# Optimization experiments

Hardware: AMD Instinct MI355X
Metric: run time of the kernel (lower is better)

The kernel has to match this reference:

```python
import jax, jax.numpy as jnp
import numpy as np

N, MAXO, IN_DIM = 4096, 16, 512
RNN_UNITS = (512, 512)
COMM_UNITS = (512, 256)
SIG = COMM_UNITS[-1]
COMM_IN = SIG + 5 + RNN_UNITS[-1]  # signal + one-hot(4) + dist + tiled features


def _lstm(x, h, c, Wx, Wh, b):
    # Keras LSTMCell gate order: i, f, g(candidate), o
    z = x @ Wx + h @ Wh + b
    i, f, g, o = jnp.split(z, 4, axis=-1)
    c2 = jax.nn.sigmoid(f) * c + jax.nn.sigmoid(i) * jnp.tanh(g)
    h2 = jax.nn.sigmoid(o) * jnp.tanh(c2)
    return h2, c2


def _mk_lstm(key, in_dim, units, scale=0.05):
    k1, k2, k3 = jax.random.split(key, 3)
    Wx = scale * jax.random.normal(k1, (in_dim, 4 * units), dtype=jnp.float32)
    Wh = scale * jax.random.normal(k2, (units, 4 * units), dtype=jnp.float32)
    b = scale * jax.random.normal(k3, (4 * units,), dtype=jnp.float32)
    return Wx, Wh, b


def setup_inputs():
    key = jax.random.key(0)
    ks = jax.random.split(key, 18)
    inputs = jax.random.normal(ks[0], (N, IN_DIM), dtype=jnp.float32)
    # interleaved triples (agent_id in [-1,N), dist, dir in [0,4))
    ids = jax.random.randint(ks[1], (N, MAXO), -1, N)
    dists = jax.random.randint(ks[2], (N, MAXO), 0, 20)
    dirs = jax.random.randint(ks[3], (N, MAXO), 0, 4)
    present_indices = jnp.stack([ids, dists, dirs], axis=2).reshape(N, 3 * MAXO).astype(jnp.int32)

    s = lambda k, shape: 0.05 * jax.random.normal(k, shape, dtype=jnp.float32)
    inp = dict(
        inputs=inputs, present_indices=present_indices,
        rnn_h1=s(ks[4], (N, RNN_UNITS[0])), rnn_c1=s(ks[5], (N, RNN_UNITS[0])),
        rnn_h2=s(ks[6], (N, RNN_UNITS[1])), rnn_c2=s(ks[7], (N, RNN_UNITS[1])),
        comm_h1=s(ks[8], (N, COMM_UNITS[0])), comm_c1=s(ks[9], (N, COMM_UNITS[0])),
        comm_h2=s(ks[10], (N, COMM_UNITS[1])), comm_c2=s(ks[11], (N, COMM_UNITS[1])),
        signals=s(ks[12], (N, SIG)),
    )
    inp['Wx1'], inp['Wh1'], inp['b1'] = _mk_lstm(ks[13], IN_DIM, RNN_UNITS[0])
    inp['Wx2'], inp['Wh2'], inp['b2'] = _mk_lstm(ks[14], RNN_UNITS[0], RNN_UNITS[1])
    inp['CWx1'], inp['CWh1'], inp['Cb1'] = _mk_lstm(ks[15], COMM_IN, COMM_UNITS[0])
    inp['CWx2'], inp['CWh2'], inp['Cb2'] = _mk_lstm(ks[16], COMM_UNITS[0], COMM_UNITS[1])
    return inp


def _forward(inputs, present_indices,
             rnn_h1, rnn_c1, rnn_h2, rnn_c2,
             comm_h1, comm_c1, comm_h2, comm_c2, signals,
             Wx1, Wh1, b1, Wx2, Wh2, b2,
             CWx1, CWh1, Cb1, CWx2, CWh2, Cb2):
    n = inputs.shape[0]
    # inner stacked LSTM step; features = output of last layer
    h1, c1 = _lstm(inputs, rnn_h1, rnn_c1, Wx1, Wh1, b1)
    h2, c2 = _lstm(h1, rnn_h2, rnn_c2, Wx2, Wh2, b2)
    features = h2  # [n, RNN_UNITS[-1]]

    vis_dists = present_indices[:, 1::3].astype(jnp.float32)      # [n, MAXO]
    vis_dirs = present_indices[:, 2::3]                            # [n, MAXO]
    pres = present_indices[:, 0::3]                                # [n, MAXO]
    dirs_onehot = jax.nn.one_hot(vis_dirs, 4, dtype=jnp.float32)   # [n, MAXO, 4]

    # append self at the end of the neighbor sequence
    pres = jnp.concatenate([pres, jnp.arange(n, dtype=pres.dtype)[:, None]], axis=1)  # [n, T]
    vis_dists = jnp.pad(vis_dists, ((0, 0), (0, 1)))
    dirs_onehot = jnp.pad(dirs_onehot, ((0, 0), (0, 1), (0, 0)))

    # _gather_present: zero row for absent (-1) neighbors
    padded_signals = jnp.pad(signals, ((1, 0), (0, 0)))            # [n+1, SIG]
    gathered = padded_signals[pres + 1]                            # [n, T, SIG]
    mask = pres >= 0                                               # [n, T]

    T = pres.shape[1]
    sig_in = jnp.concatenate([
        gathered,
        dirs_onehot,
        vis_dists[:, :, None],
        jnp.broadcast_to(features[:, None, :], (n, T, features.shape[-1])),
    ], axis=2)                                                     # [n, T, COMM_IN]

    # masked stacked-LSTM scan over the neighbor axis (Keras RNN mask semantics:
    # masked steps carry states and previous output through)
    xs = (jnp.swapaxes(sig_in, 0, 1), jnp.swapaxes(mask, 0, 1))

    def step(carry, xm):
        ch1, cc1, ch2, cc2, lo = carry
        xt, mt = xm
        nh1, nc1 = _lstm(xt, ch1, cc1, CWx1, CWh1, Cb1)
        nh2, nc2 = _lstm(nh1, ch2, cc2, CWx2, CWh2, Cb2)
        m = mt[:, None]
        carry = (jnp.where(m, nh1, ch1), jnp.where(m, nc1, cc1),
                 jnp.where(m, nh2, ch2), jnp.where(m, nc2, cc2),
                 jnp.where(m, nh2, lo))
        return carry, None

    init = (comm_h1, comm_c1, comm_h2, comm_c2, jnp.zeros_like(comm_h2))
    (nch1, ncc1, nch2, ncc2, out_signals), _ = jax.lax.scan(step, init, xs)

    full_output = jnp.concatenate([out_signals, out_signals, features], axis=1)
    return full_output


def reference(inputs, present_indices,
              rnn_h1, rnn_c1, rnn_h2, rnn_c2,
              comm_h1, comm_c1, comm_h2, comm_c2, signals,
              Wx1, Wh1, b1, Wx2, Wh2, b2,
              CWx1, CWh1, Cb1, CWx2, CWh2, Cb2):
    return _forward(inputs, present_indices,
                    rnn_h1, rnn_c1, rnn_h2, rnn_c2,
                    comm_h1, comm_c1, comm_h2, comm_c2, signals,
                    Wx1, Wh1, b1, Wx2, Wh2, b2,
                    CWx1, CWh1, Cb1, CWx2, CWh2, Cb2)
```

## Files before the change

### kernel.cpp

```cpp
#include <hip/hip_runtime.h>
#include <initializer_list>
#include <cstdint>
#include <cstddef>


typedef short short8 __attribute__((ext_vector_type(8)));
typedef float f32x4 __attribute__((ext_vector_type(4)));
typedef unsigned short us;

#define N_AG 4096

__device__ __forceinline__ us f2bf(float x) {
  unsigned int u = __float_as_uint(x);
  unsigned int r = (u + 0x7fffu + ((u >> 16) & 1u)) >> 16;
  return (us)r;
}
__device__ __forceinline__ float sigm(float x) { return 1.f / (1.f + __expf(-x)); }
__device__ __forceinline__ float tanh_f(float x) {
  float e = __expf(2.f * x);
  return 1.f - 2.f / (1.f + e);
}

struct Pair { const us* A; const us* B; int K; };
struct GemmArgs { Pair pr[6]; int np; int N; const float* base; int mode; float* C; };

typedef __attribute__((address_space(1))) const unsigned int as1u;
typedef __attribute__((address_space(3))) unsigned int as3u;
__device__ __forceinline__ void gload16(const void* g, void* l) {
  __builtin_amdgcn_global_load_lds((as1u*)g, (as3u*)l, 16, 0, 0);
}

__global__ __launch_bounds__(256) void k_gemm(GemmArgs g) {
  __shared__ __align__(16) us lA[128 * 32];
  __shared__ __align__(16) us lB[128 * 32];
  const int t = threadIdx.x;
  const int w = t >> 6, l = t & 63;
  const int bm = blockIdx.y, bn = blockIdx.x;
  const int wm = w & 1, wn = w >> 1;
  const int fr = l & 15, ks = l >> 4;
  const int srow = t >> 2;
  const int sslot = (t & 3) ^ ((srow >> 1) & 3);
  f32x4 acc[4][4] = {};

  for (int p = 0; p < g.np; ++p) {
    const us* A = g.pr[p].A;
    const us* B = g.pr[p].B;
    const int K = g.pr[p].K;
    const us* Ab = A + (size_t)bm * 128 * K;
    const us* Bb = B + (size_t)bn * 128 * K;
    for (int k0 = 0; k0 < K; k0 += 32) {
      __syncthreads();
#pragma unroll
      for (int r = 0; r < 2; ++r) {
        const int row = srow + r * 64;
        gload16(Ab + (size_t)row * K + k0 + sslot * 8, (char*)lA + r * 4096 + w * 1024);
        gload16(Bb + (size_t)row * K + k0 + sslot * 8, (char*)lB + r * 4096 + w * 1024);
      }
      __syncthreads();
      short8 af[4], bfr[4];
#pragma unroll
      for (int mi = 0; mi < 4; ++mi) {
        const int row = wm * 64 + mi * 16 + fr;
        af[mi] = *(const short8*)((const char*)lA + row * 64 + ((ks ^ ((row >> 1) & 3)) * 16));
      }
#pragma unroll
      for (int ni = 0; ni < 4; ++ni) {
        const int row = wn * 64 + ni * 16 + fr;
        bfr[ni] = *(const short8*)((const char*)lB + row * 64 + ((ks ^ ((row >> 1) & 3)) * 16));
      }
#pragma unroll
      for (int mi = 0; mi < 4; ++mi)
#pragma unroll
        for (int ni = 0; ni < 4; ++ni)
          acc[mi][ni] = __builtin_amdgcn_mfma_f32_16x16x32_bf16(af[mi], bfr[ni], acc[mi][ni], 0, 0, 0);
    }
  }
  const int N = g.N;
#pragma unroll
  for (int mi = 0; mi < 4; ++mi) {
#pragma unroll
    for (int ni = 0; ni < 4; ++ni) {
#pragma unroll
      for (int rr = 0; rr < 4; ++rr) {
        const int grow = bm * 128 + wm * 64 + mi * 16 + ks * 4 + rr;
        const int gcol = bn * 128 + wn * 64 + ni * 16 + fr;
        float v = acc[mi][ni][rr];
        if (g.mode == 1) v += g.base[gcol];
        else if (g.mode == 2) v += g.base[(size_t)grow * N + gcol];
        g.C[(size_t)grow * N + gcol] = v;
      }
    }
  }
}

__global__ __launch_bounds__(256) void k_transpose(const float* __restrict__ src,
    int Nout, int Kreal, int Kpad, int roff, us* __restrict__ dst) {
  int idx = blockIdx.x * 256 + threadIdx.x;
  if (idx >= Nout * Kpad) return;
  int no = idx % Nout;
  int k = idx / Nout;
  float v = (k < Kreal) ? src[(size_t)(roff + k) * Nout + no] : 0.f;
  dst[(size_t)no * Kpad + k] = f2bf(v);
}

__global__ __launch_bounds__(256) void k_split(const float* __restrict__ src, int n,
    float* __restrict__ f, us* __restrict__ b) {
  int idx = blockIdx.x * 256 + threadIdx.x;
  if (idx >= n) return;
  float v = src[idx];
  if (f) f[idx] = v;
  if (b) b[idx] = f2bf(v);
}

__global__ __launch_bounds__(256) void k_xvar(const int* __restrict__ pi,
    const float* __restrict__ sig, int t, us* __restrict__ xb) {
  int idx = blockIdx.x * 256 + threadIdx.x;
  if (idx >= N_AG * 288) return;
  int n = idx / 288, c = idx - n * 288;
  float v = 0.f;
  if (t < 16) {
    int p = pi[n * 48 + 3 * t];
    if (c < 256) v = (p >= 0) ? sig[(size_t)p * 256 + c] : 0.f;
    else if (c < 260) v = ((c - 256) == pi[n * 48 + 3 * t + 2]) ? 1.f : 0.f;
    else if (c == 260) v = (float)pi[n * 48 + 3 * t + 1];
  } else {
    if (c < 256) v = sig[(size_t)n * 256 + c];
  }
  xb[idx] = f2bf(v);
}

__global__ __launch_bounds__(256) void k_ew_simple(const float* __restrict__ Z,
    const float* __restrict__ cin, float* __restrict__ hf, us* __restrict__ hb) {
  int idx = blockIdx.x * 256 + threadIdx.x;
  if (idx >= N_AG * 512) return;
  int n = idx >> 9, u = idx & 511;
  const float* zr = Z + (size_t)n * 2048;
  float nc = sigm(zr[512 + u]) * cin[idx] + sigm(zr[u]) * tanh_f(zr[1024 + u]);
  float nh = sigm(zr[1536 + u]) * tanh_f(nc);
  if (hf) hf[idx] = nh;
  hb[idx] = f2bf(nh);
}

__global__ __launch_bounds__(256) void k_ew_comm1(const float* __restrict__ Z,
    const int* __restrict__ pi, int t, float* __restrict__ h, float* __restrict__ c,
    us* __restrict__ hb, us* __restrict__ nhb) {
  int idx = blockIdx.x * 256 + threadIdx.x;
  if (idx >= N_AG * 512) return;
  int n = idx >> 9, u = idx & 511;
  const float* zr = Z + (size_t)n * 2048;
  float cold = c[idx];
  float nc = sigm(zr[512 + u]) * cold + sigm(zr[u]) * tanh_f(zr[1024 + u]);
  float nh = sigm(zr[1536 + u]) * tanh_f(nc);
  bool m = (t == 16) ? true : (pi[n * 48 + 3 * t] >= 0);
  float hn = m ? nh : h[idx];
  float cn = m ? nc : cold;
  h[idx] = hn;
  c[idx] = cn;
  hb[idx] = f2bf(hn);
  nhb[idx] = f2bf(nh);
}

__global__ __launch_bounds__(256) void k_ew_comm2(const float* __restrict__ Z,
    const int* __restrict__ pi, int t, float* __restrict__ h, float* __restrict__ c,
    us* __restrict__ hb) {
  int idx = blockIdx.x * 256 + threadIdx.x;
  if (idx >= N_AG * 256) return;
  int n = idx >> 8, u = idx & 255;
  const float* zr = Z + (size_t)n * 1024;
  float cold = c[idx];
  float nc = sigm(zr[256 + u]) * cold + sigm(zr[u]) * tanh_f(zr[512 + u]);
  float nh = sigm(zr[768 + u]) * tanh_f(nc);
  bool m = (t == 16) ? true : (pi[n * 48 + 3 * t] >= 0);
  float hn = m ? nh : h[idx];
  float cn = m ? nc : cold;
  h[idx] = hn;
  c[idx] = cn;
  hb[idx] = f2bf(hn);
}

__global__ __launch_bounds__(256) void k_out(const float* __restrict__ h2,
    const float* __restrict__ feat, float* __restrict__ out) {
  int idx = blockIdx.x * 256 + threadIdx.x;
  if (idx >= N_AG * 1024) return;
  int n = idx >> 10, cc = idx & 1023;
  out[idx] = (cc < 512) ? h2[(size_t)n * 256 + (cc & 255)] : feat[(size_t)n * 512 + cc - 512];
}

extern "C" void kernel_launch(void* const* d_in, const int* in_sizes, int n_in,
                              void* d_out, int out_size, void* d_ws, size_t ws_size,
                              hipStream_t stream) {
  const float* inputs  = (const float*)d_in[0];
  const int*   pres    = (const int*)d_in[1];
  const float* rnn_h1  = (const float*)d_in[2];
  const float* rnn_c1  = (const float*)d_in[3];
  const float* rnn_h2  = (const float*)d_in[4];
  const float* rnn_c2  = (const float*)d_in[5];
  const float* comm_h1 = (const float*)d_in[6];
  const float* comm_c1 = (const float*)d_in[7];
  const float* comm_h2 = (const float*)d_in[8];
  const float* comm_c2 = (const float*)d_in[9];
  const float* signals = (const float*)d_in[10];
  const float* Wx1 = (const float*)d_in[11];
  const float* Wh1 = (const float*)d_in[12];
  const float* b1  = (const float*)d_in[13];
  const float* Wx2 = (const float*)d_in[14];
  const float* Wh2 = (const float*)d_in[15];
  const float* b2  = (const float*)d_in[16];
  const float* CWx1 = (const float*)d_in[17];
  const float* CWh1 = (const float*)d_in[18];
  const float* Cb1  = (const float*)d_in[19];
  const float* CWx2 = (const float*)d_in[20];
  const float* CWh2 = (const float*)d_in[21];
  const float* Cb2  = (const float*)d_in[22];
  float* out = (float*)d_out;
  (void)in_sizes; (void)n_in; (void)out_size;

  char* wsb = (char*)d_ws;
  size_t off = 0;
  auto alloc = [&](size_t bytes) -> char* {
    char* p = wsb + off;
    off = (off + bytes + 255) & ~(size_t)255;
    return p;
  };
  us* wx1t = (us*)alloc(2048 * 512 * 2);
  us* wh1t = (us*)alloc(2048 * 512 * 2);
  us* wx2t = (us*)alloc(2048 * 512 * 2);
  us* wh2t = (us*)alloc(2048 * 512 * 2);
  us* cx1vt = (us*)alloc(2048 * 288 * 2);
  us* cx1ft = (us*)alloc(2048 * 512 * 2);
  us* ch1t = (us*)alloc(2048 * 512 * 2);
  us* cx2t = (us*)alloc(1024 * 512 * 2);
  us* ch2t = (us*)alloc(1024 * 256 * 2);
  us* in_b  = (us*)alloc(4096 * 512 * 2);
  us* rh1_b = (us*)alloc(4096 * 512 * 2);
  us* rh2_b = (us*)alloc(4096 * 512 * 2);
  us* h1p_b = (us*)alloc(4096 * 512 * 2);
  us* ft_b  = (us*)alloc(4096 * 512 * 2);
  us* h1_b  = (us*)alloc(4096 * 512 * 2);
  us* nh1_b = (us*)alloc(4096 * 512 * 2);
  us* h2_b  = (us*)alloc(4096 * 256 * 2);
  us* xv_b  = (us*)alloc(4096 * 288 * 2);
  float* feat = (float*)alloc(4096 * 512 * 4);
  float* F1 = (float*)alloc((size_t)4096 * 2048 * 4);
  float* Z1 = (float*)alloc((size_t)4096 * 2048 * 4);
  float* Z2 = (float*)alloc((size_t)4096 * 1024 * 4);
  float* h1 = (float*)alloc(4096 * 512 * 4);
  float* c1 = (float*)alloc(4096 * 512 * 4);
  float* h2 = (float*)alloc(4096 * 256 * 4);
  float* c2 = (float*)alloc(4096 * 256 * 4);
  if (off > ws_size) return;

  auto tsp = [&](const float* src, int Nout, int Kreal, int Kpad, int roff, us* dst) {
    int tot = Nout * Kpad;
    k_transpose<<<dim3((tot + 255) / 256), dim3(256), 0, stream>>>(src, Nout, Kreal, Kpad, roff, dst);
  };
  tsp(Wx1, 2048, 512, 512, 0, wx1t);
  tsp(Wh1, 2048, 512, 512, 0, wh1t);
  tsp(Wx2, 2048, 512, 512, 0, wx2t);
  tsp(Wh2, 2048, 512, 512, 0, wh2t);
  tsp(CWx1, 2048, 261, 288, 0, cx1vt);
  tsp(CWx1, 2048, 512, 512, 261, cx1ft);
  tsp(CWh1, 2048, 512, 512, 0, ch1t);
  tsp(CWx2, 1024, 512, 512, 0, cx2t);
  tsp(CWh2, 1024, 256, 256, 0, ch2t);

  auto spl = [&](const float* src, int n, float* f, us* b) {
    k_split<<<dim3((n + 255) / 256), dim3(256), 0, stream>>>(src, n, f, b);
  };
  spl(inputs, 4096 * 512, nullptr, in_b);
  spl(rnn_h1, 4096 * 512, nullptr, rh1_b);
  spl(rnn_h2, 4096 * 512, nullptr, rh2_b);
  spl(comm_h1, 4096 * 512, h1, h1_b);
  spl(comm_c1, 4096 * 512, c1, nullptr);
  spl(comm_h2, 4096 * 256, h2, h2_b);
  spl(comm_c2, 4096 * 256, c2, nullptr);

  auto gemm = [&](std::initializer_list<Pair> ps, int Ncols, const float* base, int mode, float* C) {
    GemmArgs ga{};
    int i = 0;
    for (auto& p : ps) ga.pr[i++] = p;
    ga.np = i; ga.N = Ncols; ga.base = base; ga.mode = mode; ga.C = C;
    k_gemm<<<dim3(Ncols / 128, 4096 / 128), dim3(256), 0, stream>>>(ga);
  };

  gemm({{in_b, wx1t, 512}, {rh1_b, wh1t, 512}}, 2048, b1, 1, Z1);
  k_ew_simple<<<dim3(4096 * 512 / 256), dim3(256), 0, stream>>>(Z1, rnn_c1, nullptr, h1p_b);
  gemm({{h1p_b, wx2t, 512}, {rh2_b, wh2t, 512}}, 2048, b2, 1, Z1);
  k_ew_simple<<<dim3(4096 * 512 / 256), dim3(256), 0, stream>>>(Z1, rnn_c2, feat, ft_b);
  gemm({{ft_b, cx1ft, 512}}, 2048, Cb1, 1, F1);

  for (int t = 0; t < 17; ++t) {
    k_xvar<<<dim3((4096 * 288 + 255) / 256), dim3(256), 0, stream>>>(pres, signals, t, xv_b);
    gemm({{xv_b, cx1vt, 288}, {h1_b, ch1t, 512}}, 2048, F1, 2, Z1);
    k_ew_comm1<<<dim3(4096 * 512 / 256), dim3(256), 0, stream>>>(Z1, pres, t, h1, c1, h1_b, nh1_b);
    gemm({{nh1_b, cx2t, 512}, {h2_b, ch2t, 256}}, 1024, Cb2, 1, Z2);
    k_ew_comm2<<<dim3(4096 * 256 / 256), dim3(256), 0, stream>>>(Z2, pres, t, h2, c2, h2_b);
  }
  k_out<<<dim3(4096 * 1024 / 256), dim3(256), 0, stream>>>(h2, feat, out);
}
```

Measured before the change: 1.869 ms.

## Fuse LSTM gate elementwise into GEMM epilogue with gate-interleaved weights

Reorders weight columns so each 64-column warp tile holds the i/f/g/o gates of the same 16 units. This lets the GEMM epilogue compute the LSTM cell update directly, which removes the separate elementwise kernels and the full fp32 Z buffer round trips. The GEMM K-step also grows from 32 to 64 with a wider swizzle, and the bf16 hidden-state buffers are double-buffered so blocks can read the old state while others write the new one. The variable-input K is padded to 320, which costs a little extra compute.

```diff
diff --git a/kernel.cpp b/kernel.cpp
--- a/kernel.cpp
+++ b/kernel.cpp
@@ -22,7 +22,19 @@
 }
 
 struct Pair { const us* A; const us* B; int K; };
-struct GemmArgs { Pair pr[6]; int np; int N; const float* base; int mode; float* C; };
+struct GemmArgs {
+  Pair pr[2]; int np; int N; int nunits;
+  const float* bias;
+  const float* base2;
+  const float* cin;
+  float* cout;
+  const float* hold;
+  float* hout;
+  us* hb;
+  us* nhb;
+  const int* pres; int tt;
+  float* C; int mode;
+};
 
 typedef __attribute__((address_space(1))) const unsigned int as1u;
 typedef __attribute__((address_space(3))) unsigned int as3u;
@@ -31,15 +43,13 @@
 }
 
 __global__ __launch_bounds__(256) void k_gemm(GemmArgs g) {
-  __shared__ __align__(16) us lA[128 * 32];
-  __shared__ __align__(16) us lB[128 * 32];
+  __shared__ __align__(16) us lA[128 * 64];
+  __shared__ __align__(16) us lB[128 * 64];
   const int t = threadIdx.x;
   const int w = t >> 6, l = t & 63;
   const int bm = blockIdx.y, bn = blockIdx.x;
   const int wm = w & 1, wn = w >> 1;
   const int fr = l & 15, ks = l >> 4;
-  const int srow = t >> 2;
-  const int sslot = (t & 3) ^ ((srow >> 1) & 3);
   f32x4 acc[4][4] = {};
 
   for (int p = 0; p < g.np; ++p) {
@@ -48,59 +58,96 @@
     const int K = g.pr[p].K;
     const us* Ab = A + (size_t)bm * 128 * K;
     const us* Bb = B + (size_t)bn * 128 * K;
-    for (int k0 = 0; k0 < K; k0 += 32) {
+    for (int k0 = 0; k0 < K; k0 += 64) {
       __syncthreads();
 #pragma unroll
-      for (int r = 0; r < 2; ++r) {
-        const int row = srow + r * 64;
-        gload16(Ab + (size_t)row * K + k0 + sslot * 8, (char*)lA + r * 4096 + w * 1024);
-        gload16(Bb + (size_t)row * K + k0 + sslot * 8, (char*)lB + r * 4096 + w * 1024);
+      for (int r0 = 0; r0 < 4; ++r0) {
+        const int srow = r0 * 32 + (t >> 3);
+        const int sslot = (t & 7) ^ (srow & 7);
+        gload16(Ab + (size_t)srow * K + k0 + sslot * 8, (char*)lA + r0 * 4096 + w * 1024);
+        gload16(Bb + (size_t)srow * K + k0 + sslot * 8, (char*)lB + r0 * 4096 + w * 1024);
       }
       __syncthreads();
-      short8 af[4], bfr[4];
-#pragma unroll
-      for (int mi = 0; mi < 4; ++mi) {
-        const int row = wm * 64 + mi * 16 + fr;
-        af[mi] = *(const short8*)((const char*)lA + row * 64 + ((ks ^ ((row >> 1) & 3)) * 16));
-      }
-#pragma unroll
-      for (int ni = 0; ni < 4; ++ni) {
-        const int row = wn * 64 + ni * 16 + fr;
-        bfr[ni] = *(const short8*)((const char*)lB + row * 64 + ((ks ^ ((row >> 1) & 3)) * 16));
-      }
-#pragma unroll
-      for (int mi = 0; mi < 4; ++mi)
-#pragma unroll
-        for (int ni = 0; ni < 4; ++ni)
-          acc[mi][ni] = __builtin_amdgcn_mfma_f32_16x16x32_bf16(af[mi], bfr[ni], acc[mi][ni], 0, 0, 0);
-    }
-  }
-  const int N = g.N;
-#pragma unroll
-  for (int mi = 0; mi < 4; ++mi) {
-#pragma unroll
-    for (int ni = 0; ni < 4; ++ni) {
-#pragma unroll
-      for (int rr = 0; rr < 4; ++rr) {
-        const int grow = bm * 128 + wm * 64 + mi * 16 + ks * 4 + rr;
-        const int gcol = bn * 128 + wn * 64 + ni * 16 + fr;
-        float v = acc[mi][ni][rr];
-        if (g.mode == 1) v += g.base[gcol];
-        else if (g.mode == 2) v += g.base[(size_t)grow * N + gcol];
-        g.C[(size_t)grow * N + gcol] = v;
+#pragma unroll
+      for (int kh = 0; kh < 2; ++kh) {
+        short8 af[4], bf[4];
+#pragma unroll
+        for (int mi = 0; mi < 4; ++mi) {
+          const int row = wm * 64 + mi * 16 + fr;
+          const int s = kh * 4 + ks;
+          af[mi] = *(const short8*)((const char*)lA + row * 128 + ((s ^ (row & 7)) << 4));
+        }
+#pragma unroll
+        for (int ni = 0; ni < 4; ++ni) {
+          const int row = wn * 64 + ni * 16 + fr;
+          const int s = kh * 4 + ks;
+          bf[ni] = *(const short8*)((const char*)lB + row * 128 + ((s ^ (row & 7)) << 4));
+        }
+#pragma unroll
+        for (int mi = 0; mi < 4; ++mi)
+#pragma unroll
+          for (int ni = 0; ni < 4; ++ni)
+            acc[mi][ni] = __builtin_amdgcn_mfma_f32_16x16x32_bf16(af[mi], bf[ni], acc[mi][ni], 0, 0, 0);
       }
     }
   }
+
+  const int N = g.N, nu = g.nunits;
+  const int u = (bn * 2 + wn) * 16 + fr;
+  if (g.mode == 0) {
+#pragma unroll
+    for (int mi = 0; mi < 4; ++mi)
+#pragma unroll
+      for (int ni = 0; ni < 4; ++ni)
+#pragma unroll
+        for (int rr = 0; rr < 4; ++rr) {
+          const int grow = bm * 128 + wm * 64 + mi * 16 + ks * 4 + rr;
+          const int col = bn * 128 + wn * 64 + ni * 16 + fr;
+          g.C[(size_t)grow * N + col] = acc[mi][ni][rr] + g.bias[ni * nu + u];
+        }
+    return;
+  }
+  float bi = 0.f, bfg = 0.f, bg = 0.f, bo = 0.f;
+  if (!g.base2) { bi = g.bias[u]; bfg = g.bias[nu + u]; bg = g.bias[2 * nu + u]; bo = g.bias[3 * nu + u]; }
+#pragma unroll
+  for (int mi = 0; mi < 4; ++mi) {
+#pragma unroll
+    for (int rr = 0; rr < 4; ++rr) {
+      const int grow = bm * 128 + wm * 64 + mi * 16 + ks * 4 + rr;
+      float zi = acc[mi][0][rr], zf = acc[mi][1][rr], zg = acc[mi][2][rr], zo = acc[mi][3][rr];
+      if (g.base2) {
+        const float* fb = g.base2 + (size_t)grow * N + bn * 128 + wn * 64 + fr;
+        zi += fb[0]; zf += fb[16]; zg += fb[32]; zo += fb[48];
+      } else {
+        zi += bi; zf += bfg; zg += bg; zo += bo;
+      }
+      const size_t off = (size_t)grow * nu + u;
+      const float cold = g.cin[off];
+      const float nc = sigm(zf) * cold + sigm(zi) * tanh_f(zg);
+      const float nh = sigm(zo) * tanh_f(nc);
+      bool m = true;
+      if (g.tt >= 0 && g.tt < 16) m = (g.pres[grow * 48 + 3 * g.tt] >= 0);
+      const float cn = m ? nc : cold;
+      float hn = nh;
+      if (g.hold) hn = m ? nh : g.hold[off];
+      if (g.cout) g.cout[off] = cn;
+      if (g.hout) g.hout[off] = hn;
+      g.hb[off] = f2bf(hn);
+      if (g.nhb) g.nhb[off] = f2bf(nh);
+    }
+  }
 }
 
 __global__ __launch_bounds__(256) void k_transpose(const float* __restrict__ src,
-    int Nout, int Kreal, int Kpad, int roff, us* __restrict__ dst) {
+    int Nout, int nunits, int Kreal, int Kpad, int roff, us* __restrict__ dst) {
   int idx = blockIdx.x * 256 + threadIdx.x;
   if (idx >= Nout * Kpad) return;
-  int no = idx % Nout;
+  int col = idx % Nout;
   int k = idx / Nout;
-  float v = (k < Kreal) ? src[(size_t)(roff + k) * Nout + no] : 0.f;
-  dst[(size_t)no * Kpad + k] = f2bf(v);
+  int gate = (col >> 4) & 3;
+  int u = ((col >> 6) << 4) | (col & 15);
+  float v = (k < Kreal) ? src[(size_t)(roff + k) * Nout + gate * nunits + u] : 0.f;
+  dst[(size_t)col * Kpad + k] = f2bf(v);
 }
 
 __global__ __launch_bounds__(256) void k_split(const float* __restrict__ src, int n,
@@ -115,8 +162,8 @@
 __global__ __launch_bounds__(256) void k_xvar(const int* __restrict__ pi,
     const float* __restrict__ sig, int t, us* __restrict__ xb) {
   int idx = blockIdx.x * 256 + threadIdx.x;
-  if (idx >= N_AG * 288) return;
-  int n = idx / 288, c = idx - n * 288;
+  if (idx >= N_AG * 320) return;
+  int n = idx / 320, c = idx - n * 320;
   float v = 0.f;
   if (t < 16) {
     int p = pi[n * 48 + 3 * t];
@@ -127,55 +174,6 @@
     if (c < 256) v = sig[(size_t)n * 256 + c];
   }
   xb[idx] = f2bf(v);
-}
-
-__global__ __launch_bounds__(256) void k_ew_simple(const float* __restrict__ Z,
-    const float* __restrict__ cin, float* __restrict__ hf, us* __restrict__ hb) {
-  int idx = blockIdx.x * 256 + threadIdx.x;
-  if (idx >= N_AG * 512) return;
-  int n = idx >> 9, u = idx & 511;
-  const float* zr = Z + (size_t)n * 2048;
-  float nc = sigm(zr[512 + u]) * cin[idx] + sigm(zr[u]) * tanh_f(zr[1024 + u]);
-  float nh = sigm(zr[1536 + u]) * tanh_f(nc);
-  if (hf) hf[idx] = nh;
-  hb[idx] = f2bf(nh);
-}
-
-__global__ __launch_bounds__(256) void k_ew_comm1(const float* __restrict__ Z,
-    const int* __restrict__ pi, int t, float* __restrict__ h, float* __restrict__ c,
-    us* __restrict__ hb, us* __restrict__ nhb) {
-  int idx = blockIdx.x * 256 + threadIdx.x;
-  if (idx >= N_AG * 512) return;
-  int n = idx >> 9, u = idx & 511;
-  const float* zr = Z + (size_t)n * 2048;
-  float cold = c[idx];
-  float nc = sigm(zr[512 + u]) * cold + sigm(zr[u]) * tanh_f(zr[1024 + u]);
-  float nh = sigm(zr[1536 + u]) * tanh_f(nc);
-  bool m = (t == 16) ? true : (pi[n * 48 + 3 * t] >= 0);
-  float hn = m ? nh : h[idx];
-  float cn = m ? nc : cold;
-  h[idx] = hn;
-  c[idx] = cn;
-  hb[idx] = f2bf(hn);
-  nhb[idx] = f2bf(nh);
-}
-
-__global__ __launch_bounds__(256) void k_ew_comm2(const float* __restrict__ Z,
-    const int* __restrict__ pi, int t, float* __restrict__ h, float* __restrict__ c,
-    us* __restrict__ hb) {
-  int idx = blockIdx.x * 256 + threadIdx.x;
-  if (idx >= N_AG * 256) return;
-  int n = idx >> 8, u = idx & 255;
-  const float* zr = Z + (size_t)n * 1024;
-  float cold = c[idx];
-  float nc = sigm(zr[256 + u]) * cold + sigm(zr[u]) * tanh_f(zr[512 + u]);
-  float nh = sigm(zr[768 + u]) * tanh_f(nc);
-  bool m = (t == 16) ? true : (pi[n * 48 + 3 * t] >= 0);
-  float hn = m ? nh : h[idx];
-  float cn = m ? nc : cold;
-  h[idx] = hn;
-  c[idx] = cn;
-  hb[idx] = f2bf(hn);
 }
 
 __global__ __launch_bounds__(256) void k_out(const float* __restrict__ h2,
@@ -222,28 +220,28 @@
     off = (off + bytes + 255) & ~(size_t)255;
     return p;
   };
-  us* wx1t = (us*)alloc(2048 * 512 * 2);
-  us* wh1t = (us*)alloc(2048 * 512 * 2);
-  us* wx2t = (us*)alloc(2048 * 512 * 2);
-  us* wh2t = (us*)alloc(2048 * 512 * 2);
-  us* cx1vt = (us*)alloc(2048 * 288 * 2);
+  us* wx1t  = (us*)alloc(2048 * 512 * 2);
+  us* wh1t  = (us*)alloc(2048 * 512 * 2);
+  us* wx2t  = (us*)alloc(2048 * 512 * 2);
+  us* wh2t  = (us*)alloc(2048 * 512 * 2);
+  us* cx1vt = (us*)alloc(2048 * 320 * 2);
   us* cx1ft = (us*)alloc(2048 * 512 * 2);
-  us* ch1t = (us*)alloc(2048 * 512 * 2);
-  us* cx2t = (us*)alloc(1024 * 512 * 2);
-  us* ch2t = (us*)alloc(1024 * 256 * 2);
-  us* in_b  = (us*)alloc(4096 * 512 * 2);
-  us* rh1_b = (us*)alloc(4096 * 512 * 2);
-  us* rh2_b = (us*)alloc(4096 * 512 * 2);
-  us* h1p_b = (us*)alloc(4096 * 512 * 2);
-  us* ft_b  = (us*)alloc(4096 * 512 * 2);
-  us* h1_b  = (us*)alloc(4096 * 512 * 2);
-  us* nh1_b = (us*)alloc(4096 * 512 * 2);
-  us* h2_b  = (us*)alloc(4096 * 256 * 2);
-  us* xv_b  = (us*)alloc(4096 * 288 * 2);
+  us* ch1t  = (us*)alloc(2048 * 512 * 2);
+  us* cx2t  = (us*)alloc(1024 * 512 * 2);
+  us* ch2t  = (us*)alloc(1024 * 256 * 2);
+  us* in_b   = (us*)alloc(4096 * 512 * 2);
+  us* rh1_b  = (us*)alloc(4096 * 512 * 2);
+  us* rh2_b  = (us*)alloc(4096 * 512 * 2);
+  us* h1p_b  = (us*)alloc(4096 * 512 * 2);
+  us* ft_b   = (us*)alloc(4096 * 512 * 2);
+  us* h1b0   = (us*)alloc(4096 * 512 * 2);
+  us* h1b1   = (us*)alloc(4096 * 512 * 2);
+  us* nh1_b  = (us*)alloc(4096 * 512 * 2);
+  us* h2b0   = (us*)alloc(4096 * 256 * 2);
+  us* h2b1   = (us*)alloc(4096 * 256 * 2);
+  us* xv_b   = (us*)alloc(4096 * 320 * 2);
   float* feat = (float*)alloc(4096 * 512 * 4);
-  float* F1 = (float*)alloc((size_t)4096 * 2048 * 4);
-  float* Z1 = (float*)alloc((size_t)4096 * 2048 * 4);
-  float* Z2 = (float*)alloc((size_t)4096 * 1024 * 4);
+  float* F1   = (float*)alloc((size_t)4096 * 2048 * 4);
   float* h1 = (float*)alloc(4096 * 512 * 4);
   float* c1 = (float*)alloc(4096 * 512 * 4);
   float* h2 = (float*)alloc(4096 * 256 * 4);
@@ -252,13 +250,13 @@
 
   auto tsp = [&](const float* src, int Nout, int Kreal, int Kpad, int roff, us* dst) {
     int tot = Nout * Kpad;
-    k_transpose<<<dim3((tot + 255) / 256), dim3(256), 0, stream>>>(src, Nout, Kreal, Kpad, roff, dst);
+    k_transpose<<<dim3((tot + 255) / 256), dim3(256), 0, stream>>>(src, Nout, Nout / 4, Kreal, Kpad, roff, dst);
   };
   tsp(Wx1, 2048, 512, 512, 0, wx1t);
   tsp(Wh1, 2048, 512, 512, 0, wh1t);
   tsp(Wx2, 2048, 512, 512, 0, wx2t);
   tsp(Wh2, 2048, 512, 512, 0, wh2t);
-  tsp(CWx1, 2048, 261, 288, 0, cx1vt);
+  tsp(CWx1, 2048, 261, 320, 0, cx1vt);
   tsp(CWx1, 2048, 512, 512, 261, cx1ft);
   tsp(CWh1, 2048, 512, 512, 0, ch1t);
   tsp(CWx2, 1024, 512, 512, 0, cx2t);
@@ -270,31 +268,50 @@
   spl(inputs, 4096 * 512, nullptr, in_b);
   spl(rnn_h1, 4096 * 512, nullptr, rh1_b);
   spl(rnn_h2, 4096 * 512, nullptr, rh2_b);
-  spl(comm_h1, 4096 * 512, h1, h1_b);
+  spl(comm_h1, 4096 * 512, h1, h1b0);
   spl(comm_c1, 4096 * 512, c1, nullptr);
-  spl(comm_h2, 4096 * 256, h2, h2_b);
+  spl(comm_h2, 4096 * 256, h2, h2b0);
   spl(comm_c2, 4096 * 256, c2, nullptr);
 
-  auto gemm = [&](std::initializer_list<Pair> ps, int Ncols, const float* base, int mode, float* C) {
+  auto launch = [&](GemmArgs& ga) {
+    k_gemm<<<dim3(ga.N / 128, 4096 / 128), dim3(256), 0, stream>>>(ga);
+  };
+  auto lstm = [&](std::initializer_list<Pair> ps, int Ncols, const float* bias, const float* base2,
+                  const float* cin, float* cout, const float* hold, float* hout,
+                  us* hb, us* nhb, const int* pm, int tt) {
     GemmArgs ga{};
     int i = 0;
     for (auto& p : ps) ga.pr[i++] = p;
-    ga.np = i; ga.N = Ncols; ga.base = base; ga.mode = mode; ga.C = C;
-    k_gemm<<<dim3(Ncols / 128, 4096 / 128), dim3(256), 0, stream>>>(ga);
-  };
-
-  gemm({{in_b, wx1t, 512}, {rh1_b, wh1t, 512}}, 2048, b1, 1, Z1);
-  k_ew_simple<<<dim3(4096 * 512 / 256), dim3(256), 0, stream>>>(Z1, rnn_c1, nullptr, h1p_b);
-  gemm({{h1p_b, wx2t, 512}, {rh2_b, wh2t, 512}}, 2048, b2, 1, Z1);
-  k_ew_simple<<<dim3(4096 * 512 / 256), dim3(256), 0, stream>>>(Z1, rnn_c2, feat, ft_b);
-  gemm({{ft_b, cx1ft, 512}}, 2048, Cb1, 1, F1);
-
+    ga.np = i; ga.N = Ncols; ga.nunits = Ncols / 4;
+    ga.bias = bias; ga.base2 = base2; ga.cin = cin; ga.cout = cout;
+    ga.hold = hold; ga.hout = hout; ga.hb = hb; ga.nhb = nhb;
+    ga.pres = pm; ga.tt = tt; ga.C = nullptr; ga.mode = 1;
+    launch(ga);
+  };
+  auto plain = [&](std::initializer_list<Pair> ps, int Ncols, const float* bias, float* C) {
+    GemmArgs ga{};
+    int i = 0;
+    for (auto& p : ps) ga.pr[i++] = p;
+    ga.np = i; ga.N = Ncols; ga.nunits = Ncols / 4;
+    ga.bias = bias; ga.C = C; ga.mode = 0; ga.tt = -1;
+    launch(ga);
+  };
+
+  lstm({{in_b, wx1t, 512}, {rh1_b, wh1t, 512}}, 2048, b1, nullptr,
+       rnn_c1, nullptr, nullptr, nullptr, h1p_b, nullptr, nullptr, -1);
+  lstm({{h1p_b, wx2t, 512}, {rh2_b, wh2t, 512}}, 2048, b2, nullptr,
+       rnn_c2, nullptr, nullptr, feat, ft_b, nullptr, nullptr, -1);
+  plain({{ft_b, cx1ft, 512}}, 2048, Cb1, F1);
+
+  us* h1bp[2] = {h1b0, h1b1};
+  us* h2bp[2] = {h2b0, h2b1};
   for (int t = 0; t < 17; ++t) {
-    k_xvar<<<dim3((4096 * 288 + 255) / 256), dim3(256), 0, stream>>>(pres, signals, t, xv_b);
-    gemm({{xv_b, cx1vt, 288}, {h1_b, ch1t, 512}}, 2048, F1, 2, Z1);
-    k_ew_comm1<<<dim3(4096 * 512 / 256), dim3(256), 0, stream>>>(Z1, pres, t, h1, c1, h1_b, nh1_b);
-    gemm({{nh1_b, cx2t, 512}, {h2_b, ch2t, 256}}, 1024, Cb2, 1, Z2);
-    k_ew_comm2<<<dim3(4096 * 256 / 256), dim3(256), 0, stream>>>(Z2, pres, t, h2, c2, h2_b);
+    const int rd = t & 1, wr = rd ^ 1;
+    k_xvar<<<dim3((4096 * 320 + 255) / 256), dim3(256), 0, stream>>>(pres, signals, t, xv_b);
+    lstm({{xv_b, cx1vt, 320}, {h1bp[rd], ch1t, 512}}, 2048, nullptr, F1,
+         c1, c1, h1, h1, h1bp[wr], nh1_b, pres, t);
+    lstm({{nh1_b, cx2t, 512}, {h2bp[rd], ch2t, 256}}, 1024, Cb2, nullptr,
+         c2, c2, h2, h2, h2bp[wr], nullptr, pres, t);
   }
   k_out<<<dim3(4096 * 1024 / 256), dim3(256), 0, stream>>>(h2, feat, out);
 }
```

New measurement: 1.504 ms. 19.5% less time.
